# Performance work log

Hardware: AMD Instinct MI355X
Metric: run time of the kernel (lower is better)

Reference implementation:

```python
import jax, jax.numpy as jnp
import numpy as np

B, S, H = 2, 2048, 1024
NH = 16
HD = H // NH


def setup_inputs() -> dict:
    key = jax.random.key(0)
    ks = jax.random.split(key, 9)
    std = 1.0 / np.sqrt(H)
    inp = {"x": jax.random.normal(ks[0], (B, S, H), dtype=jnp.float32)}
    names = ["Wq", "Wk", "Wv", "Wo"]
    for i, n in enumerate(names):
        inp[n] = jax.random.uniform(ks[1 + i], (H, H), dtype=jnp.float32, minval=-std, maxval=std)
        inp["b" + n[1:]] = jax.random.uniform(ks[5 + i], (H,), dtype=jnp.float32, minval=-std, maxval=std)
    return inp


def reference(x, Wq, Wk, Wv, Wo, bq, bk, bv, bo):
    scale = HD ** -0.5
    # projections: torch Linear is x @ W.T + b
    def proj(W, b):
        y = jnp.einsum('bsh,oh->bso', x, W) + b
        return y.reshape(B, S, NH, HD).transpose(0, 2, 1, 3)  # [B, NH, S, HD]
    Q = proj(Wq, bq)
    K = proj(Wk, bk)
    V = proj(Wv, bv)
    scores = jnp.einsum('bhqd,bhkd->bhqk', Q, K) * scale  # [B, NH, S, S]
    attn = jax.nn.softmax(scores, axis=-1)
    ctx = jnp.einsum('bhqk,bhkd->bhqd', attn, V)
    ctx = ctx.transpose(0, 2, 1, 3).reshape(B, S, H)
    out = jnp.einsum('bsh,oh->bso', ctx, Wo) + bo
    avg_attention = attn.mean(axis=1).mean(axis=1)  # [B, S] (mean over heads, then query dim)
    return out, avg_attention
```

## Files before the change

### kernel.cpp

```cpp
#include <hip/hip_runtime.h>
#include <hip/hip_bf16.h>

#define B_  2
#define S_  2048
#define H_  1024
#define NH_ 16
#define HD_ 64
#define NTOK (B_*S_)

typedef __attribute__((ext_vector_type(8))) short bf16x8;
typedef __attribute__((ext_vector_type(4))) float f32x4;

static __device__ __forceinline__ ushort f2bf(float f) {
    __hip_bfloat16 h = __float2bfloat16(f);
    return *reinterpret_cast<ushort*>(&h);
}

static __device__ __forceinline__ void gload_lds16(const void* g, void* l) {
    __builtin_amdgcn_global_load_lds(
        (const __attribute__((address_space(1))) void*)g,
        (__attribute__((address_space(3))) void*)l,
        16, 0, 0);
}

__global__ __launch_bounds__(256) void f32_to_bf16(
    const float* __restrict__ s, ushort* __restrict__ d, int n8)
{
    const int i = blockIdx.x * 256 + threadIdx.x;
    if (i >= n8) return;
    const float4 a = reinterpret_cast<const float4*>(s)[2*i + 0];
    const float4 b = reinterpret_cast<const float4*>(s)[2*i + 1];
    ushort u[8];
    u[0] = f2bf(a.x); u[1] = f2bf(a.y); u[2] = f2bf(a.z); u[3] = f2bf(a.w);
    u[4] = f2bf(b.x); u[5] = f2bf(b.y); u[6] = f2bf(b.z); u[7] = f2bf(b.w);
    reinterpret_cast<uint4*>(d)[i] = *reinterpret_cast<uint4*>(u);
}

struct Cvt4 { const float* s[4]; ushort* d[4]; };
__global__ __launch_bounds__(256) void w_to_bf16(Cvt4 a, int n8)
{
    const int z = blockIdx.y;
    const int i = blockIdx.x * 256 + threadIdx.x;
    if (i >= n8) return;
    const float* s = a.s[z];
    const float4 va = reinterpret_cast<const float4*>(s)[2*i + 0];
    const float4 vb = reinterpret_cast<const float4*>(s)[2*i + 1];
    ushort u[8];
    u[0] = f2bf(va.x); u[1] = f2bf(va.y); u[2] = f2bf(va.z); u[3] = f2bf(va.w);
    u[4] = f2bf(vb.x); u[5] = f2bf(vb.y); u[6] = f2bf(vb.z); u[7] = f2bf(vb.w);
    reinterpret_cast<uint4*>(a.d[z])[i] = *reinterpret_cast<uint4*>(u);
}

__global__ __launch_bounds__(256) void transpose_v(
    const ushort* __restrict__ Vb, ushort* __restrict__ Vt)
{
    __shared__ ushort T[64][72];
    const int t  = threadIdx.x;
    const int b  = blockIdx.z;
    const int h  = blockIdx.y;
    const int s0 = blockIdx.x * 64;
    const int r  = t >> 2;
    const int c0 = (t & 3) * 16;

    const ushort* src = Vb + (size_t)(b*S_ + s0 + r)*H_ + h*HD_ + c0;
    *reinterpret_cast<uint4*>(&T[r][c0])     = *reinterpret_cast<const uint4*>(src);
    *reinterpret_cast<uint4*>(&T[r][c0 + 8]) = *reinterpret_cast<const uint4*>(src + 8);
    __syncthreads();

    const int d = r;
    ushort tmp[16];
#pragma unroll
    for (int k = 0; k < 16; ++k) tmp[k] = T[c0 + k][d];
    ushort* dst = Vt + ((size_t)((b*NH_ + h)*HD_ + d))*S_ + s0 + c0;
    *reinterpret_cast<uint4*>(dst)     = *reinterpret_cast<uint4*>(&tmp[0]);
    *reinterpret_cast<uint4*>(dst + 8) = *reinterpret_cast<uint4*>(&tmp[8]);
}

struct GemmArgs {
    const ushort* W[3];
    const float*  bias[3];
    void*         Y[3];
};

template<int MREP, bool BF16OUT>
__global__ __launch_bounds__(256) void gemm_mfma_bt(
    const ushort* __restrict__ A, GemmArgs args, int M, int N, int K)
{
    constexpr int BM = MREP * 32;
    __shared__ __align__(16) ushort As[BM * 64];
    __shared__ __align__(16) ushort Bs[128 * 64];

    const int z = blockIdx.z;
    const ushort* __restrict__ W   = args.W[z];
    const float*  __restrict__ bia = args.bias[z];

    const int t  = threadIdx.x;
    const int w  = t >> 6;
    const int l  = t & 63;
    const int lq = l >> 4;
    const int ln = l & 15;
    const int wr = w >> 1;
    const int wc = w & 1;
    const int m0 = blockIdx.x * BM;
    const int n0 = blockIdx.y * 128;
    const int srow = l >> 3;
    const int scol = (l & 7) * 8;

    f32x4 acc[MREP][4];
#pragma unroll
    for (int m = 0; m < MREP; ++m)
#pragma unroll
        for (int n = 0; n < 4; ++n) acc[m][n] = f32x4{0.f, 0.f, 0.f, 0.f};

    for (int k0 = 0; k0 < K; k0 += 64) {
        __syncthreads();
#pragma unroll
        for (int i = 0; i < BM/32; ++i) {
            const int rb = i*32 + w*8;
            gload_lds16(A + (size_t)(m0 + rb + srow)*K + k0 + scol, &As[rb*64]);
        }
#pragma unroll
        for (int i = 0; i < 4; ++i) {
            const int rb = i*32 + w*8;
            gload_lds16(W + (size_t)(n0 + rb + srow)*K + k0 + scol, &Bs[rb*64]);
        }
        __syncthreads();
#pragma unroll
        for (int ks = 0; ks < 2; ++ks) {
            bf16x8 bfr[4];
#pragma unroll
            for (int n = 0; n < 4; ++n)
                bfr[n] = *reinterpret_cast<const bf16x8*>(&Bs[(wc*64 + n*16 + ln)*64 + ks*32 + lq*8]);
#pragma unroll
            for (int m = 0; m < MREP; ++m) {
                const bf16x8 afr = *reinterpret_cast<const bf16x8*>(&As[(wr*MREP*16 + m*16 + ln)*64 + ks*32 + lq*8]);
#pragma unroll
                for (int n = 0; n < 4; ++n)
                    acc[m][n] = __builtin_amdgcn_mfma_f32_16x16x32_bf16(afr, bfr[n], acc[m][n], 0, 0, 0);
            }
        }
    }

    float bv[4];
#pragma unroll
    for (int n = 0; n < 4; ++n) bv[n] = bia[n0 + wc*64 + n*16 + ln];

#pragma unroll
    for (int m = 0; m < MREP; ++m) {
#pragma unroll
        for (int r = 0; r < 4; ++r) {
            const size_t row = (size_t)(m0 + wr*MREP*16 + m*16 + lq*4 + r);
#pragma unroll
            for (int n = 0; n < 4; ++n) {
                const int col = n0 + wc*64 + n*16 + ln;
                const float val = acc[m][n][r] + bv[n];
                if constexpr (BF16OUT)
                    ((ushort*)args.Y[z])[row*N + col] = f2bf(val);
                else
                    ((float*)args.Y[z])[row*N + col] = val;
            }
        }
    }
}

__global__ __launch_bounds__(256) void attn_pv(
    const ushort* __restrict__ Qb, const ushort* __restrict__ Kb,
    const ushort* __restrict__ Vtg, ushort* __restrict__ ctx,
    float* __restrict__ invl_g)
{
    __shared__ __align__(16) ushort Ks[64*64];
    __shared__ __align__(16) ushort Vs[64*64];
    __shared__ __align__(16) ushort Ps[4][16][72];

    const int t  = threadIdx.x;
    const int w  = t >> 6;
    const int l  = t & 63;
    const int lq = l >> 4;
    const int ln = l & 15;
    const int b  = blockIdx.z;
    const int h  = blockIdx.y;
    const int q0 = blockIdx.x * 64;
    const float scale = 0.125f;

    bf16x8 qf[2];
    {
        const ushort* qrow = Qb + ((size_t)(b*S_ + q0 + w*16 + ln))*H_ + h*HD_ + lq*8;
        qf[0] = *reinterpret_cast<const bf16x8*>(qrow);
        qf[1] = *reinterpret_cast<const bf16x8*>(qrow + 32);
    }

    size_t koff[2], voff[2];
    int    dsto[2];
#pragma unroll
    for (int i = 0; i < 2; ++i) {
        const int chunk = i*256 + w*64 + l;
        const int row   = chunk >> 3;
        const int c8    = (chunk & 7) ^ (row & 7);
        koff[i] = (size_t)(b*S_ + row)*H_ + h*HD_ + c8*8;
        voff[i] = ((size_t)((b*NH_ + h)*HD_ + row))*S_ + c8*8;
        dsto[i] = (i*256 + w*64)*8;
    }

    float lsum[4] = {0.f, 0.f, 0.f, 0.f};
    f32x4 oacc[4];
#pragma unroll
    for (int nt = 0; nt < 4; ++nt) oacc[nt] = f32x4{0.f, 0.f, 0.f, 0.f};

    for (int kt = 0; kt < S_; kt += 64) {
        __syncthreads();
#pragma unroll
        for (int i = 0; i < 2; ++i)
            gload_lds16(Kb + koff[i] + (size_t)kt*H_, &Ks[dsto[i]]);
#pragma unroll
        for (int i = 0; i < 2; ++i)
            gload_lds16(Vtg + voff[i] + kt, &Vs[dsto[i]]);
        __syncthreads();

        f32x4 sacc[4];
#pragma unroll
        for (int nt = 0; nt < 4; ++nt) sacc[nt] = f32x4{0.f, 0.f, 0.f, 0.f};
#pragma unroll
        for (int ks = 0; ks < 2; ++ks) {
#pragma unroll
            for (int nt = 0; nt < 4; ++nt) {
                const bf16x8 kb = *reinterpret_cast<const bf16x8*>(
                    &Ks[(nt*16 + ln)*64 + (((ks*4 + lq) ^ (ln & 7)) * 8)]);
                sacc[nt] = __builtin_amdgcn_mfma_f32_16x16x32_bf16(qf[ks], kb, sacc[nt], 0, 0, 0);
            }
        }

#pragma unroll
        for (int nt = 0; nt < 4; ++nt) {
#pragma unroll
            for (int r = 0; r < 4; ++r) {
                const float e = __expf(sacc[nt][r] * scale);
                lsum[r] += e;
                Ps[w][lq*4 + r][nt*16 + ln] = f2bf(e);
            }
        }

#pragma unroll
        for (int ks = 0; ks < 2; ++ks) {
            const bf16x8 pa = *reinterpret_cast<const bf16x8*>(&Ps[w][ln][ks*32 + lq*8]);
#pragma unroll
            for (int nt = 0; nt < 4; ++nt) {
                const bf16x8 vb8 = *reinterpret_cast<const bf16x8*>(
                    &Vs[(nt*16 + ln)*64 + (((ks*4 + lq) ^ (ln & 7)) * 8)]);
                oacc[nt] = __builtin_amdgcn_mfma_f32_16x16x32_bf16(pa, vb8, oacc[nt], 0, 0, 0);
            }
        }
    }

    float invl[4];
#pragma unroll
    for (int r = 0; r < 4; ++r) {
        lsum[r] += __shfl_xor(lsum[r], 1);
        lsum[r] += __shfl_xor(lsum[r], 2);
        lsum[r] += __shfl_xor(lsum[r], 4);
        lsum[r] += __shfl_xor(lsum[r], 8);
        invl[r] = 1.f / lsum[r];
    }

    if (ln == 0) {
        float* dst = invl_g + (size_t)(b*NH_ + h)*S_ + q0 + w*16 + lq*4;
#pragma unroll
        for (int r = 0; r < 4; ++r) dst[r] = invl[r];
    }

    ushort* crow = ctx + ((size_t)(b*S_ + q0 + w*16 + lq*4))*H_ + h*HD_ + ln;
#pragma unroll
    for (int r = 0; r < 4; ++r)
#pragma unroll
        for (int nt = 0; nt < 4; ++nt)
            crow[(size_t)r*H_ + nt*16] = f2bf(oacc[nt][r] * invl[r]);
}

__global__ __launch_bounds__(256) void attn_colsum(
    const ushort* __restrict__ Qb, const ushort* __restrict__ Kb,
    const float* __restrict__ invl_g, float* __restrict__ colsum)
{
    __shared__ __align__(16) ushort KsT[64*64];
    __shared__ __align__(16) ushort Qs[64*64];
    __shared__ __align__(16) float  iv[S_];

    const int t  = threadIdx.x;
    const int w  = t >> 6;
    const int l  = t & 63;
    const int lq = l >> 4;
    const int ln = l & 15;
    const int b  = blockIdx.z;
    const int h  = blockIdx.y;
    const int k0 = blockIdx.x * 64;
    const int bh = b*NH_ + h;
    const float scale = 0.125f;

    int chunkrow[2], chunkc8[2], dsto[2];
#pragma unroll
    for (int i = 0; i < 2; ++i) {
        const int chunk = i*256 + w*64 + l;
        chunkrow[i] = chunk >> 3;
        chunkc8[i]  = (chunk & 7) ^ (chunkrow[i] & 7);
        dsto[i]     = (i*256 + w*64)*8;
    }

#pragma unroll
    for (int i = 0; i < 2; ++i) {
        const int chunk = i*256 + w*64 + l;
        gload_lds16(invl_g + (size_t)bh*S_ + chunk*4, &iv[(i*256 + w*64)*4]);
        gload_lds16(Kb + (size_t)(b*S_ + k0 + chunkrow[i])*H_ + h*HD_ + chunkc8[i]*8,
                    &KsT[dsto[i]]);
    }
    __syncthreads();

    bf16x8 kf[2];
#pragma unroll
    for (int ks = 0; ks < 2; ++ks)
        kf[ks] = *reinterpret_cast<const bf16x8*>(
            &KsT[(w*16 + ln)*64 + (((ks*4 + lq) ^ (ln & 7)) * 8)]);

    float cs = 0.f;

    for (int qt = 0; qt < S_; qt += 64) {
        __syncthreads();
#pragma unroll
        for (int i = 0; i < 2; ++i)
            gload_lds16(Qb + (size_t)(b*S_ + qt + chunkrow[i])*H_ + h*HD_ + chunkc8[i]*8,
                        &Qs[dsto[i]]);
        __syncthreads();

#pragma unroll
        for (int c = 0; c < 4; ++c) {
            f32x4 sacc = f32x4{0.f, 0.f, 0.f, 0.f};
#pragma unroll
            for (int ks = 0; ks < 2; ++ks) {
                const bf16x8 af = *reinterpret_cast<const bf16x8*>(
                    &Qs[(c*16 + ln)*64 + (((ks*4 + lq) ^ (ln & 7)) * 8)]);
                sacc = __builtin_amdgcn_mfma_f32_16x16x32_bf16(af, kf[ks], sacc, 0, 0, 0);
            }
            const f32x4 iv4 = *reinterpret_cast<const f32x4*>(&iv[qt + c*16 + lq*4]);
#pragma unroll
            for (int r = 0; r < 4; ++r)
                cs += __expf(sacc[r] * scale) * iv4[r];
        }
    }

    cs += __shfl_xor(cs, 16);
    cs += __shfl_xor(cs, 32);
    if (l < 16)
        atomicAdd(&colsum[(size_t)b*S_ + k0 + w*16 + l], cs);
}

__global__ void zero_f32(float* p, int n)
{
    const int i = blockIdx.x * 256 + threadIdx.x;
    if (i < n) p[i] = 0.f;
}

__global__ void avg_write(const float* __restrict__ colsum, float* __restrict__ out, float inv)
{
    const int i = blockIdx.x * 256 + threadIdx.x;
    if (i < NTOK) out[i] = colsum[i] * inv;
}

extern "C" void kernel_launch(void* const* d_in, const int* in_sizes, int n_in,
                              void* d_out, int out_size, void* d_ws, size_t ws_size,
                              hipStream_t stream)
{
    const float* x  = (const float*)d_in[0];
    const float* Wq = (const float*)d_in[1];
    const float* bq = (const float*)d_in[2];
    const float* Wk = (const float*)d_in[3];
    const float* bk = (const float*)d_in[4];
    const float* Wv = (const float*)d_in[5];
    const float* bv = (const float*)d_in[6];
    const float* Wo = (const float*)d_in[7];
    const float* bo = (const float*)d_in[8];

    float* out     = (float*)d_out;
    float* avg_out = out + (size_t)NTOK * H_;

    char* ws = (char*)d_ws;
    const size_t mat  = (size_t)NTOK * H_ * sizeof(ushort);
    const size_t wmat = (size_t)H_ * H_ * sizeof(ushort);
    ushort* xb   = (ushort*)(ws);
    ushort* Qb   = (ushort*)(ws + mat);
    ushort* Kb   = (ushort*)(ws + 2*mat);
    ushort* Vb   = (ushort*)(ws + 3*mat);
    ushort* Vtg  = (ushort*)(ws + 4*mat);
    ushort* Wqb  = (ushort*)(ws + 5*mat);
    ushort* Wkb  = (ushort*)(ws + 5*mat + wmat);
    ushort* Wvb  = (ushort*)(ws + 5*mat + 2*wmat);
    ushort* Wob  = (ushort*)(ws + 5*mat + 3*wmat);
    float*  colsum = (float*)(ws + 5*mat + 4*wmat);
    float*  invl   = (float*)(ws + 5*mat + 4*wmat + 64*1024);
    ushort* ctxb = xb;

    const dim3 blk(256);

    f32_to_bf16<<<dim3((NTOK*H_/8 + 255)/256), blk, 0, stream>>>(x, xb, NTOK*H_/8);
    {
        Cvt4 c;
        c.s[0] = Wq; c.s[1] = Wk; c.s[2] = Wv; c.s[3] = Wo;
        c.d[0] = Wqb; c.d[1] = Wkb; c.d[2] = Wvb; c.d[3] = Wob;
        w_to_bf16<<<dim3((H_*H_/8 + 255)/256, 4), blk, 0, stream>>>(c, H_*H_/8);
    }

    zero_f32<<<dim3((NTOK + 255)/256), blk, 0, stream>>>(colsum, NTOK);

    {
        GemmArgs ga;
        ga.W[0] = Wqb; ga.W[1] = Wkb; ga.W[2] = Wvb;
        ga.bias[0] = bq; ga.bias[1] = bk; ga.bias[2] = bv;
        ga.Y[0] = Qb; ga.Y[1] = Kb; ga.Y[2] = Vb;
        gemm_mfma_bt<4, true><<<dim3(NTOK/128, H_/128, 3), blk, 0, stream>>>(
            xb, ga, NTOK, H_, H_);
    }

    transpose_v<<<dim3(S_/64, NH_, B_), blk, 0, stream>>>(Vb, Vtg);

    const dim3 gattn(S_/64, NH_, B_);
    attn_pv<<<gattn, blk, 0, stream>>>(Qb, Kb, Vtg, ctxb, invl);
    attn_colsum<<<gattn, blk, 0, stream>>>(Qb, Kb, invl, colsum);

    {
        GemmArgs ga;
        ga.W[0] = Wob; ga.W[1] = Wob; ga.W[2] = Wob;
        ga.bias[0] = bo; ga.bias[1] = bo; ga.bias[2] = bo;
        ga.Y[0] = out; ga.Y[1] = out; ga.Y[2] = out;
        gemm_mfma_bt<2, false><<<dim3(NTOK/64, H_/128, 1), blk, 0, stream>>>(
            ctxb, ga, NTOK, H_, H_);
    }

    avg_write<<<dim3((NTOK + 255)/256), blk, 0, stream>>>(colsum, avg_out, 1.f/((float)NH_ * (float)S_));
}
```

Baseline: 203.8 us.

## Double per-wave query/key tiles in attention kernels and use exp2 scaling

Both attention kernels now process 128 rows per block instead of 64: each wave handles two 16-row query (or key) sub-tiles, so each K/V tile loaded into shared memory is reused across twice as many MFMAs. The S computation swaps operand order so the P tile can be written to shared memory as packed 4-element vectors, and row sums are reduced with fewer shuffles. exp is computed as exp2f with a prescaled constant. This halves the grid to 512 blocks, which may reduce occupancy and latency hiding, and raises register pressure.

```diff
diff --git a/kernel.cpp b/kernel.cpp
--- a/kernel.cpp
+++ b/kernel.cpp
@@ -10,6 +10,8 @@
 
 typedef __attribute__((ext_vector_type(8))) short bf16x8;
 typedef __attribute__((ext_vector_type(4))) float f32x4;
+
+#define SC2 0.18033688011112042f
 
 static __device__ __forceinline__ ushort f2bf(float f) {
     __hip_bfloat16 h = __float2bfloat16(f);
@@ -170,7 +172,7 @@
 {
     __shared__ __align__(16) ushort Ks[64*64];
     __shared__ __align__(16) ushort Vs[64*64];
-    __shared__ __align__(16) ushort Ps[4][16][72];
+    __shared__ __align__(16) ushort Ps[4][32][72];
 
     const int t  = threadIdx.x;
     const int w  = t >> 6;
@@ -179,32 +181,34 @@
     const int ln = l & 15;
     const int b  = blockIdx.z;
     const int h  = blockIdx.y;
-    const int q0 = blockIdx.x * 64;
-    const float scale = 0.125f;
-
-    bf16x8 qf[2];
-    {
-        const ushort* qrow = Qb + ((size_t)(b*S_ + q0 + w*16 + ln))*H_ + h*HD_ + lq*8;
-        qf[0] = *reinterpret_cast<const bf16x8*>(qrow);
-        qf[1] = *reinterpret_cast<const bf16x8*>(qrow + 32);
+    const int q0 = blockIdx.x * 128;
+
+    bf16x8 qf[2][2];
+#pragma unroll
+    for (int qs = 0; qs < 2; ++qs) {
+        const ushort* qrow = Qb + ((size_t)(b*S_ + q0 + w*32 + qs*16 + ln))*H_ + h*HD_ + lq*8;
+        qf[qs][0] = *reinterpret_cast<const bf16x8*>(qrow);
+        qf[qs][1] = *reinterpret_cast<const bf16x8*>(qrow + 32);
     }
 
     size_t koff[2], voff[2];
     int    dsto[2];
 #pragma unroll
     for (int i = 0; i < 2; ++i) {
-        const int chunk = i*256 + w*64 + l;
+        const int chunk = i*256 + t;
         const int row   = chunk >> 3;
         const int c8    = (chunk & 7) ^ (row & 7);
         koff[i] = (size_t)(b*S_ + row)*H_ + h*HD_ + c8*8;
         voff[i] = ((size_t)((b*NH_ + h)*HD_ + row))*S_ + c8*8;
-        dsto[i] = (i*256 + w*64)*8;
-    }
-
-    float lsum[4] = {0.f, 0.f, 0.f, 0.f};
-    f32x4 oacc[4];
-#pragma unroll
-    for (int nt = 0; nt < 4; ++nt) oacc[nt] = f32x4{0.f, 0.f, 0.f, 0.f};
+        dsto[i] = chunk*8;
+    }
+
+    float lsum[2] = {0.f, 0.f};
+    f32x4 oacc[2][4];
+#pragma unroll
+    for (int qs = 0; qs < 2; ++qs)
+#pragma unroll
+        for (int nt = 0; nt < 4; ++nt) oacc[qs][nt] = f32x4{0.f, 0.f, 0.f, 0.f};
 
     for (int kt = 0; kt < S_; kt += 64) {
         __syncthreads();
@@ -216,70 +220,93 @@
             gload_lds16(Vtg + voff[i] + kt, &Vs[dsto[i]]);
         __syncthreads();
 
-        f32x4 sacc[4];
-#pragma unroll
-        for (int nt = 0; nt < 4; ++nt) sacc[nt] = f32x4{0.f, 0.f, 0.f, 0.f};
+        f32x4 sacc[2][4];
+#pragma unroll
+        for (int qs = 0; qs < 2; ++qs)
+#pragma unroll
+            for (int nt = 0; nt < 4; ++nt) sacc[qs][nt] = f32x4{0.f, 0.f, 0.f, 0.f};
 #pragma unroll
         for (int ks = 0; ks < 2; ++ks) {
+            bf16x8 kb[4];
+#pragma unroll
+            for (int nt = 0; nt < 4; ++nt)
+                kb[nt] = *reinterpret_cast<const bf16x8*>(
+                    &Ks[(nt*16 + ln)*64 + (((ks*4 + lq) ^ (ln & 7)) * 8)]);
+#pragma unroll
+            for (int qs = 0; qs < 2; ++qs)
+#pragma unroll
+                for (int nt = 0; nt < 4; ++nt)
+                    sacc[qs][nt] = __builtin_amdgcn_mfma_f32_16x16x32_bf16(
+                        kb[nt], qf[qs][ks], sacc[qs][nt], 0, 0, 0);
+        }
+
+#pragma unroll
+        for (int qs = 0; qs < 2; ++qs) {
 #pragma unroll
             for (int nt = 0; nt < 4; ++nt) {
-                const bf16x8 kb = *reinterpret_cast<const bf16x8*>(
-                    &Ks[(nt*16 + ln)*64 + (((ks*4 + lq) ^ (ln & 7)) * 8)]);
-                sacc[nt] = __builtin_amdgcn_mfma_f32_16x16x32_bf16(qf[ks], kb, sacc[nt], 0, 0, 0);
+                ushort pk[4];
+#pragma unroll
+                for (int r = 0; r < 4; ++r) {
+                    const float e = exp2f(sacc[qs][nt][r] * SC2);
+                    lsum[qs] += e;
+                    pk[r] = f2bf(e);
+                }
+                *reinterpret_cast<uint2*>(&Ps[w][qs*16 + ln][nt*16 + lq*4]) =
+                    *reinterpret_cast<uint2*>(pk);
             }
         }
 
 #pragma unroll
-        for (int nt = 0; nt < 4; ++nt) {
-#pragma unroll
-            for (int r = 0; r < 4; ++r) {
-                const float e = __expf(sacc[nt][r] * scale);
-                lsum[r] += e;
-                Ps[w][lq*4 + r][nt*16 + ln] = f2bf(e);
-            }
-        }
-
-#pragma unroll
         for (int ks = 0; ks < 2; ++ks) {
-            const bf16x8 pa = *reinterpret_cast<const bf16x8*>(&Ps[w][ln][ks*32 + lq*8]);
+            bf16x8 pa[2];
+#pragma unroll
+            for (int qs = 0; qs < 2; ++qs)
+                pa[qs] = *reinterpret_cast<const bf16x8*>(&Ps[w][qs*16 + ln][ks*32 + lq*8]);
 #pragma unroll
             for (int nt = 0; nt < 4; ++nt) {
                 const bf16x8 vb8 = *reinterpret_cast<const bf16x8*>(
                     &Vs[(nt*16 + ln)*64 + (((ks*4 + lq) ^ (ln & 7)) * 8)]);
-                oacc[nt] = __builtin_amdgcn_mfma_f32_16x16x32_bf16(pa, vb8, oacc[nt], 0, 0, 0);
+#pragma unroll
+                for (int qs = 0; qs < 2; ++qs)
+                    oacc[qs][nt] = __builtin_amdgcn_mfma_f32_16x16x32_bf16(
+                        pa[qs], vb8, oacc[qs][nt], 0, 0, 0);
             }
         }
     }
 
-    float invl[4];
-#pragma unroll
-    for (int r = 0; r < 4; ++r) {
-        lsum[r] += __shfl_xor(lsum[r], 1);
-        lsum[r] += __shfl_xor(lsum[r], 2);
-        lsum[r] += __shfl_xor(lsum[r], 4);
-        lsum[r] += __shfl_xor(lsum[r], 8);
-        invl[r] = 1.f / lsum[r];
-    }
-
-    if (ln == 0) {
-        float* dst = invl_g + (size_t)(b*NH_ + h)*S_ + q0 + w*16 + lq*4;
-#pragma unroll
-        for (int r = 0; r < 4; ++r) dst[r] = invl[r];
-    }
-
-    ushort* crow = ctx + ((size_t)(b*S_ + q0 + w*16 + lq*4))*H_ + h*HD_ + ln;
-#pragma unroll
-    for (int r = 0; r < 4; ++r)
-#pragma unroll
-        for (int nt = 0; nt < 4; ++nt)
-            crow[(size_t)r*H_ + nt*16] = f2bf(oacc[nt][r] * invl[r]);
+    float invl[2];
+#pragma unroll
+    for (int qs = 0; qs < 2; ++qs) {
+        lsum[qs] += __shfl_xor(lsum[qs], 16);
+        lsum[qs] += __shfl_xor(lsum[qs], 32);
+        invl[qs] = 1.f / lsum[qs];
+    }
+
+    if (lq == 0) {
+#pragma unroll
+        for (int qs = 0; qs < 2; ++qs)
+            invl_g[(size_t)(b*NH_ + h)*S_ + q0 + w*32 + qs*16 + ln] = invl[qs];
+    }
+
+#pragma unroll
+    for (int qs = 0; qs < 2; ++qs) {
+        float ivr[4];
+#pragma unroll
+        for (int r = 0; r < 4; ++r) ivr[r] = __shfl(invl[qs], lq*4 + r);
+        ushort* crow = ctx + ((size_t)(b*S_ + q0 + w*32 + qs*16 + lq*4))*H_ + h*HD_ + ln;
+#pragma unroll
+        for (int r = 0; r < 4; ++r)
+#pragma unroll
+            for (int nt = 0; nt < 4; ++nt)
+                crow[(size_t)r*H_ + nt*16] = f2bf(oacc[qs][nt][r] * ivr[r]);
+    }
 }
 
 __global__ __launch_bounds__(256) void attn_colsum(
     const ushort* __restrict__ Qb, const ushort* __restrict__ Kb,
     const float* __restrict__ invl_g, float* __restrict__ colsum)
 {
-    __shared__ __align__(16) ushort KsT[64*64];
+    __shared__ __align__(16) ushort KsT[128*64];
     __shared__ __align__(16) ushort Qs[64*64];
     __shared__ __align__(16) float  iv[S_];
 
@@ -290,64 +317,81 @@
     const int ln = l & 15;
     const int b  = blockIdx.z;
     const int h  = blockIdx.y;
-    const int k0 = blockIdx.x * 64;
+    const int k0 = blockIdx.x * 128;
     const int bh = b*NH_ + h;
-    const float scale = 0.125f;
-
-    int chunkrow[2], chunkc8[2], dsto[2];
+
+#pragma unroll
+    for (int i = 0; i < 4; ++i) {
+        const int chunk = i*256 + t;
+        const int row   = chunk >> 3;
+        const int c8    = (chunk & 7) ^ (row & 7);
+        gload_lds16(Kb + (size_t)(b*S_ + k0 + row)*H_ + h*HD_ + c8*8, &KsT[chunk*8]);
+    }
 #pragma unroll
     for (int i = 0; i < 2; ++i) {
-        const int chunk = i*256 + w*64 + l;
-        chunkrow[i] = chunk >> 3;
-        chunkc8[i]  = (chunk & 7) ^ (chunkrow[i] & 7);
-        dsto[i]     = (i*256 + w*64)*8;
-    }
-
+        const int chunk = i*256 + t;
+        gload_lds16(invl_g + (size_t)bh*S_ + chunk*4, &iv[chunk*4]);
+    }
+
+    int qrow[2], qc8[2];
 #pragma unroll
     for (int i = 0; i < 2; ++i) {
-        const int chunk = i*256 + w*64 + l;
-        gload_lds16(invl_g + (size_t)bh*S_ + chunk*4, &iv[(i*256 + w*64)*4]);
-        gload_lds16(Kb + (size_t)(b*S_ + k0 + chunkrow[i])*H_ + h*HD_ + chunkc8[i]*8,
-                    &KsT[dsto[i]]);
-    }
+        const int chunk = i*256 + t;
+        qrow[i] = chunk >> 3;
+        qc8[i]  = (chunk & 7) ^ (qrow[i] & 7);
+    }
+
     __syncthreads();
 
-    bf16x8 kf[2];
-#pragma unroll
-    for (int ks = 0; ks < 2; ++ks)
-        kf[ks] = *reinterpret_cast<const bf16x8*>(
-            &KsT[(w*16 + ln)*64 + (((ks*4 + lq) ^ (ln & 7)) * 8)]);
-
-    float cs = 0.f;
+    bf16x8 kf[2][2];
+#pragma unroll
+    for (int sub = 0; sub < 2; ++sub)
+#pragma unroll
+        for (int ks = 0; ks < 2; ++ks)
+            kf[sub][ks] = *reinterpret_cast<const bf16x8*>(
+                &KsT[(w*32 + sub*16 + ln)*64 + (((ks*4 + lq) ^ (ln & 7)) * 8)]);
+
+    float cs[2] = {0.f, 0.f};
 
     for (int qt = 0; qt < S_; qt += 64) {
         __syncthreads();
 #pragma unroll
         for (int i = 0; i < 2; ++i)
-            gload_lds16(Qb + (size_t)(b*S_ + qt + chunkrow[i])*H_ + h*HD_ + chunkc8[i]*8,
-                        &Qs[dsto[i]]);
+            gload_lds16(Qb + (size_t)(b*S_ + qt + qrow[i])*H_ + h*HD_ + qc8[i]*8,
+                        &Qs[(i*256 + t)*8]);
         __syncthreads();
 
 #pragma unroll
         for (int c = 0; c < 4; ++c) {
-            f32x4 sacc = f32x4{0.f, 0.f, 0.f, 0.f};
+            f32x4 sacc[2] = {f32x4{0.f,0.f,0.f,0.f}, f32x4{0.f,0.f,0.f,0.f}};
 #pragma unroll
             for (int ks = 0; ks < 2; ++ks) {
                 const bf16x8 af = *reinterpret_cast<const bf16x8*>(
                     &Qs[(c*16 + ln)*64 + (((ks*4 + lq) ^ (ln & 7)) * 8)]);
-                sacc = __builtin_amdgcn_mfma_f32_16x16x32_bf16(af, kf[ks], sacc, 0, 0, 0);
+#pragma unroll
+                for (int sub = 0; sub < 2; ++sub)
+                    sacc[sub] = __builtin_amdgcn_mfma_f32_16x16x32_bf16(
+                        af, kf[sub][ks], sacc[sub], 0, 0, 0);
             }
             const f32x4 iv4 = *reinterpret_cast<const f32x4*>(&iv[qt + c*16 + lq*4]);
 #pragma unroll
-            for (int r = 0; r < 4; ++r)
-                cs += __expf(sacc[r] * scale) * iv4[r];
-        }
-    }
-
-    cs += __shfl_xor(cs, 16);
-    cs += __shfl_xor(cs, 32);
-    if (l < 16)
-        atomicAdd(&colsum[(size_t)b*S_ + k0 + w*16 + l], cs);
+            for (int sub = 0; sub < 2; ++sub)
+#pragma unroll
+                for (int r = 0; r < 4; ++r)
+                    cs[sub] += exp2f(sacc[sub][r] * SC2) * iv4[r];
+        }
+    }
+
+#pragma unroll
+    for (int sub = 0; sub < 2; ++sub) {
+        cs[sub] += __shfl_xor(cs[sub], 16);
+        cs[sub] += __shfl_xor(cs[sub], 32);
+    }
+    if (l < 16) {
+#pragma unroll
+        for (int sub = 0; sub < 2; ++sub)
+            atomicAdd(&colsum[(size_t)b*S_ + k0 + w*32 + sub*16 + l], cs[sub]);
+    }
 }
 
 __global__ void zero_f32(float* p, int n)
@@ -418,9 +462,8 @@
 
     transpose_v<<<dim3(S_/64, NH_, B_), blk, 0, stream>>>(Vb, Vtg);
 
-    const dim3 gattn(S_/64, NH_, B_);
-    attn_pv<<<gattn, blk, 0, stream>>>(Qb, Kb, Vtg, ctxb, invl);
-    attn_colsum<<<gattn, blk, 0, stream>>>(Qb, Kb, invl, colsum);
+    attn_pv<<<dim3(S_/128, NH_, B_), blk, 0, stream>>>(Qb, Kb, Vtg, ctxb, invl);
+    attn_colsum<<<dim3(S_/128, NH_, B_), blk, 0, stream>>>(Qb, Kb, invl, colsum);
 
     {
         GemmArgs ga;
```

After: 221.5 us. +8.7%, slower.

## Double-buffer K/Q tiles in attention kernels and fold normalizer into exp2

Applied to the files above, without the earlier changes.

Both attention kernels now double-buffer the streamed K (attn_pv) or Q (attn_colsum) tile in LDS and prefetch the next tile while computing the current one, using explicit vmcnt waits and a raw barrier. The score MFMA operands are swapped so each lane holds a query column, which reduces row sums to a scalar, packs P stores as bf16 pairs, and uses exp2 with a pre-multiplied log2e scale. attn_pv stores -log2(l) instead of 1/l, so colsum can fold the normalization into a single fma+exp2. The goal is to hide global-load latency and trim ALU and LDS store work, at the cost of more LDS and hand-managed synchronisation.

```diff
diff --git a/kernel.cpp b/kernel.cpp
--- a/kernel.cpp
+++ b/kernel.cpp
@@ -11,9 +11,15 @@
 typedef __attribute__((ext_vector_type(8))) short bf16x8;
 typedef __attribute__((ext_vector_type(4))) float f32x4;
 
+#define SC2 0.18033688011112042f
+
 static __device__ __forceinline__ ushort f2bf(float f) {
     __hip_bfloat16 h = __float2bfloat16(f);
     return *reinterpret_cast<ushort*>(&h);
+}
+static __device__ __forceinline__ uint f2bf2(float lo, float hi) {
+    __hip_bfloat162 v = __float22bfloat162_rn(float2{lo, hi});
+    return *reinterpret_cast<uint*>(&v);
 }
 
 static __device__ __forceinline__ void gload_lds16(const void* g, void* l) {
@@ -166,9 +172,9 @@
 __global__ __launch_bounds__(256) void attn_pv(
     const ushort* __restrict__ Qb, const ushort* __restrict__ Kb,
     const ushort* __restrict__ Vtg, ushort* __restrict__ ctx,
-    float* __restrict__ invl_g)
-{
-    __shared__ __align__(16) ushort Ks[64*64];
+    float* __restrict__ il2_g)
+{
+    __shared__ __align__(16) ushort Ks[2][64*64];
     __shared__ __align__(16) ushort Vs[64*64];
     __shared__ __align__(16) ushort Ps[4][16][72];
 
@@ -180,7 +186,6 @@
     const int b  = blockIdx.z;
     const int h  = blockIdx.y;
     const int q0 = blockIdx.x * 64;
-    const float scale = 0.125f;
 
     bf16x8 qf[2];
     {
@@ -193,51 +198,71 @@
     int    dsto[2];
 #pragma unroll
     for (int i = 0; i < 2; ++i) {
-        const int chunk = i*256 + w*64 + l;
+        const int chunk = i*256 + t;
         const int row   = chunk >> 3;
         const int c8    = (chunk & 7) ^ (row & 7);
         koff[i] = (size_t)(b*S_ + row)*H_ + h*HD_ + c8*8;
         voff[i] = ((size_t)((b*NH_ + h)*HD_ + row))*S_ + c8*8;
-        dsto[i] = (i*256 + w*64)*8;
-    }
-
-    float lsum[4] = {0.f, 0.f, 0.f, 0.f};
+        dsto[i] = chunk*8;
+    }
+
+    float lsum = 0.f;
     f32x4 oacc[4];
 #pragma unroll
     for (int nt = 0; nt < 4; ++nt) oacc[nt] = f32x4{0.f, 0.f, 0.f, 0.f};
 
+#pragma unroll
+    for (int i = 0; i < 2; ++i)
+        gload_lds16(Kb + koff[i], &Ks[0][dsto[i]]);
+    __syncthreads();
+
+    int cur = 0;
     for (int kt = 0; kt < S_; kt += 64) {
-        __syncthreads();
-#pragma unroll
-        for (int i = 0; i < 2; ++i)
-            gload_lds16(Kb + koff[i] + (size_t)kt*H_, &Ks[dsto[i]]);
 #pragma unroll
         for (int i = 0; i < 2; ++i)
             gload_lds16(Vtg + voff[i] + kt, &Vs[dsto[i]]);
-        __syncthreads();
-
+        const bool pre = (kt + 64 < S_);
+        if (pre) {
+#pragma unroll
+            for (int i = 0; i < 2; ++i)
+                gload_lds16(Kb + koff[i] + (size_t)(kt + 64)*H_, &Ks[cur ^ 1][dsto[i]]);
+        }
+
+        const ushort* ksb = &Ks[cur][0];
         f32x4 sacc[4];
 #pragma unroll
         for (int nt = 0; nt < 4; ++nt) sacc[nt] = f32x4{0.f, 0.f, 0.f, 0.f};
 #pragma unroll
         for (int ks = 0; ks < 2; ++ks) {
-#pragma unroll
-            for (int nt = 0; nt < 4; ++nt) {
-                const bf16x8 kb = *reinterpret_cast<const bf16x8*>(
-                    &Ks[(nt*16 + ln)*64 + (((ks*4 + lq) ^ (ln & 7)) * 8)]);
-                sacc[nt] = __builtin_amdgcn_mfma_f32_16x16x32_bf16(qf[ks], kb, sacc[nt], 0, 0, 0);
+            bf16x8 kb[4];
+#pragma unroll
+            for (int nt = 0; nt < 4; ++nt)
+                kb[nt] = *reinterpret_cast<const bf16x8*>(
+                    &ksb[(nt*16 + ln)*64 + (((ks*4 + lq) ^ (ln & 7)) * 8)]);
+#pragma unroll
+            for (int nt = 0; nt < 4; ++nt)
+                sacc[nt] = __builtin_amdgcn_mfma_f32_16x16x32_bf16(
+                    kb[nt], qf[ks], sacc[nt], 0, 0, 0);
+        }
+
+#pragma unroll
+        for (int nt = 0; nt < 4; ++nt) {
+            float e[4];
+#pragma unroll
+            for (int r = 0; r < 4; ++r) {
+                e[r] = exp2f(sacc[nt][r] * SC2);
+                lsum += e[r];
             }
-        }
-
-#pragma unroll
-        for (int nt = 0; nt < 4; ++nt) {
-#pragma unroll
-            for (int r = 0; r < 4; ++r) {
-                const float e = __expf(sacc[nt][r] * scale);
-                lsum[r] += e;
-                Ps[w][lq*4 + r][nt*16 + ln] = f2bf(e);
-            }
-        }
+            uint2 pk;
+            pk.x = f2bf2(e[0], e[1]);
+            pk.y = f2bf2(e[2], e[3]);
+            *reinterpret_cast<uint2*>(&Ps[w][ln][nt*16 + lq*4]) = pk;
+        }
+
+        if (pre) asm volatile("s_waitcnt vmcnt(2)" ::: "memory");
+        else     asm volatile("s_waitcnt vmcnt(0)" ::: "memory");
+        __builtin_amdgcn_s_barrier();
+        __builtin_amdgcn_sched_barrier(0);
 
 #pragma unroll
         for (int ks = 0; ks < 2; ++ks) {
@@ -246,41 +271,39 @@
             for (int nt = 0; nt < 4; ++nt) {
                 const bf16x8 vb8 = *reinterpret_cast<const bf16x8*>(
                     &Vs[(nt*16 + ln)*64 + (((ks*4 + lq) ^ (ln & 7)) * 8)]);
-                oacc[nt] = __builtin_amdgcn_mfma_f32_16x16x32_bf16(pa, vb8, oacc[nt], 0, 0, 0);
+                oacc[nt] = __builtin_amdgcn_mfma_f32_16x16x32_bf16(
+                    pa, vb8, oacc[nt], 0, 0, 0);
             }
         }
-    }
-
-    float invl[4];
-#pragma unroll
-    for (int r = 0; r < 4; ++r) {
-        lsum[r] += __shfl_xor(lsum[r], 1);
-        lsum[r] += __shfl_xor(lsum[r], 2);
-        lsum[r] += __shfl_xor(lsum[r], 4);
-        lsum[r] += __shfl_xor(lsum[r], 8);
-        invl[r] = 1.f / lsum[r];
-    }
-
-    if (ln == 0) {
-        float* dst = invl_g + (size_t)(b*NH_ + h)*S_ + q0 + w*16 + lq*4;
-#pragma unroll
-        for (int r = 0; r < 4; ++r) dst[r] = invl[r];
-    }
-
+
+        __syncthreads();
+        cur ^= 1;
+    }
+
+    lsum += __shfl_xor(lsum, 16);
+    lsum += __shfl_xor(lsum, 32);
+    const float invl = 1.f / lsum;
+
+    if (lq == 0)
+        il2_g[(size_t)(b*NH_ + h)*S_ + q0 + w*16 + ln] = -__log2f(lsum);
+
+    float ivr[4];
+#pragma unroll
+    for (int r = 0; r < 4; ++r) ivr[r] = __shfl(invl, lq*4 + r);
     ushort* crow = ctx + ((size_t)(b*S_ + q0 + w*16 + lq*4))*H_ + h*HD_ + ln;
 #pragma unroll
     for (int r = 0; r < 4; ++r)
 #pragma unroll
         for (int nt = 0; nt < 4; ++nt)
-            crow[(size_t)r*H_ + nt*16] = f2bf(oacc[nt][r] * invl[r]);
+            crow[(size_t)r*H_ + nt*16] = f2bf(oacc[nt][r] * ivr[r]);
 }
 
 __global__ __launch_bounds__(256) void attn_colsum(
     const ushort* __restrict__ Qb, const ushort* __restrict__ Kb,
-    const float* __restrict__ invl_g, float* __restrict__ colsum)
+    const float* __restrict__ il2_g, float* __restrict__ colsum)
 {
     __shared__ __align__(16) ushort KsT[64*64];
-    __shared__ __align__(16) ushort Qs[64*64];
+    __shared__ __align__(16) ushort Qs[2][64*64];
     __shared__ __align__(16) float  iv[S_];
 
     const int t  = threadIdx.x;
@@ -292,23 +315,21 @@
     const int h  = blockIdx.y;
     const int k0 = blockIdx.x * 64;
     const int bh = b*NH_ + h;
-    const float scale = 0.125f;
-
-    int chunkrow[2], chunkc8[2], dsto[2];
+
+    int crow_[2], cc8[2], dsto[2];
 #pragma unroll
     for (int i = 0; i < 2; ++i) {
-        const int chunk = i*256 + w*64 + l;
-        chunkrow[i] = chunk >> 3;
-        chunkc8[i]  = (chunk & 7) ^ (chunkrow[i] & 7);
-        dsto[i]     = (i*256 + w*64)*8;
+        const int chunk = i*256 + t;
+        crow_[i] = chunk >> 3;
+        cc8[i]   = (chunk & 7) ^ (crow_[i] & 7);
+        dsto[i]  = chunk*8;
     }
 
 #pragma unroll
     for (int i = 0; i < 2; ++i) {
-        const int chunk = i*256 + w*64 + l;
-        gload_lds16(invl_g + (size_t)bh*S_ + chunk*4, &iv[(i*256 + w*64)*4]);
-        gload_lds16(Kb + (size_t)(b*S_ + k0 + chunkrow[i])*H_ + h*HD_ + chunkc8[i]*8,
-                    &KsT[dsto[i]]);
+        gload_lds16(Kb + (size_t)(b*S_ + k0 + crow_[i])*H_ + h*HD_ + cc8[i]*8, &KsT[dsto[i]]);
+        gload_lds16(il2_g + (size_t)bh*S_ + (i*256 + t)*4, &iv[(i*256 + t)*4]);
+        gload_lds16(Qb + (size_t)(b*S_ + crow_[i])*H_ + h*HD_ + cc8[i]*8, &Qs[0][dsto[i]]);
     }
     __syncthreads();
 
@@ -320,13 +341,15 @@
 
     float cs = 0.f;
 
+    int cur = 0;
     for (int qt = 0; qt < S_; qt += 64) {
-        __syncthreads();
-#pragma unroll
-        for (int i = 0; i < 2; ++i)
-            gload_lds16(Qb + (size_t)(b*S_ + qt + chunkrow[i])*H_ + h*HD_ + chunkc8[i]*8,
-                        &Qs[dsto[i]]);
-        __syncthreads();
+        if (qt + 64 < S_) {
+#pragma unroll
+            for (int i = 0; i < 2; ++i)
+                gload_lds16(Qb + (size_t)(b*S_ + qt + 64 + crow_[i])*H_ + h*HD_ + cc8[i]*8,
+                            &Qs[cur ^ 1][dsto[i]]);
+        }
+        const ushort* qsb = &Qs[cur][0];
 
 #pragma unroll
         for (int c = 0; c < 4; ++c) {
@@ -334,14 +357,17 @@
 #pragma unroll
             for (int ks = 0; ks < 2; ++ks) {
                 const bf16x8 af = *reinterpret_cast<const bf16x8*>(
-                    &Qs[(c*16 + ln)*64 + (((ks*4 + lq) ^ (ln & 7)) * 8)]);
+                    &qsb[(c*16 + ln)*64 + (((ks*4 + lq) ^ (ln & 7)) * 8)]);
                 sacc = __builtin_amdgcn_mfma_f32_16x16x32_bf16(af, kf[ks], sacc, 0, 0, 0);
             }
             const f32x4 iv4 = *reinterpret_cast<const f32x4*>(&iv[qt + c*16 + lq*4]);
 #pragma unroll
             for (int r = 0; r < 4; ++r)
-                cs += __expf(sacc[r] * scale) * iv4[r];
-        }
+                cs += exp2f(fmaf(sacc[r], SC2, iv4[r]));
+        }
+
+        __syncthreads();
+        cur ^= 1;
     }
 
     cs += __shfl_xor(cs, 16);
@@ -392,7 +418,7 @@
     ushort* Wvb  = (ushort*)(ws + 5*mat + 2*wmat);
     ushort* Wob  = (ushort*)(ws + 5*mat + 3*wmat);
     float*  colsum = (float*)(ws + 5*mat + 4*wmat);
-    float*  invl   = (float*)(ws + 5*mat + 4*wmat + 64*1024);
+    float*  il2    = (float*)(ws + 5*mat + 4*wmat + 64*1024);
     ushort* ctxb = xb;
 
     const dim3 blk(256);
@@ -418,9 +444,8 @@
 
     transpose_v<<<dim3(S_/64, NH_, B_), blk, 0, stream>>>(Vb, Vtg);
 
-    const dim3 gattn(S_/64, NH_, B_);
-    attn_pv<<<gattn, blk, 0, stream>>>(Qb, Kb, Vtg, ctxb, invl);
-    attn_colsum<<<gattn, blk, 0, stream>>>(Qb, Kb, invl, colsum);
+    attn_pv<<<dim3(S_/64, NH_, B_), blk, 0, stream>>>(Qb, Kb, Vtg, ctxb, il2);
+    attn_colsum<<<dim3(S_/64, NH_, B_), blk, 0, stream>>>(Qb, Kb, il2, colsum);
 
     {
         GemmArgs ga;
```

Result: slower. 210.9 us (+3.5%).
